# Optimization experiments

Hardware: AMD Instinct MI355X
Metric: run time of the kernel (lower is better)

## Reference

```python
import jax, jax.numpy as jnp
import numpy as np

D_MODEL = 1024
N_HEAD = 16
HEAD_DIM = D_MODEL // N_HEAD


def setup_inputs() -> dict:
    key = jax.random.key(0)
    k1, k2, k3 = jax.random.split(key, 3)
    B, T = 2, 2048
    s = 1.0 / np.sqrt(D_MODEL)
    return {
        "x": jax.random.normal(k1, (B, T, D_MODEL), dtype=jnp.float32),
        "w_qkv": jax.random.normal(k2, (D_MODEL, 3 * D_MODEL), dtype=jnp.float32) * s,
        "b_qkv": jnp.zeros((3 * D_MODEL,), dtype=jnp.float32),
        "w_out": jax.random.normal(k3, (D_MODEL, D_MODEL), dtype=jnp.float32) * s,
        "b_out": jnp.zeros((D_MODEL,), dtype=jnp.float32),
    }


def reference(x, w_qkv, b_qkv, w_out, b_out):
    B, T, C = x.shape
    qkv = x @ w_qkv + b_qkv                      # [B,T,3C]
    q, k, v = jnp.split(qkv, 3, axis=-1)
    # [B,T,C] -> [B,H,T,hd]
    def to_heads(t):
        return t.reshape(B, T, N_HEAD, HEAD_DIM).transpose(0, 2, 1, 3)
    q, k, v = to_heads(q), to_heads(k), to_heads(v)
    scale = 1.0 / np.sqrt(HEAD_DIM).astype(np.float32)
    att = jnp.einsum("bhqd,bhkd->bhqk", q, k) * scale  # [B,H,T,T]
    causal = jnp.tril(jnp.ones((T, T), dtype=bool))
    att = jnp.where(causal, att, -jnp.inf)
    att = jax.nn.softmax(att, axis=-1)
    y = jnp.einsum("bhqk,bhkd->bhqd", att, v)    # [B,H,T,hd]
    y = y.transpose(0, 2, 1, 3).reshape(B, T, C)
    return y @ w_out + b_out
```

## Files before the change

### kernel.cpp

```cpp
#include <hip/hip_runtime.h>
#include <stdint.h>

#define D_MODEL 1024
#define NHEAD 16
#define HD 64
#define BB 2
#define TT 2048
#define MR (BB*TT)

#define SCL2 0.18033688011112042f

typedef unsigned short u16;
typedef __bf16 bf16x8 __attribute__((ext_vector_type(8)));
typedef __bf16 bf16x4v __attribute__((ext_vector_type(4)));
typedef u16 u16x8 __attribute__((ext_vector_type(8)));
typedef float f32x4 __attribute__((ext_vector_type(4)));

__device__ __forceinline__ u16 f2bf(float f) {
  union { float f; unsigned u; } v; v.f = f;
  unsigned r = v.u + 0x7FFFu + ((v.u >> 16) & 1u);
  return (u16)(r >> 16);
}

__device__ __forceinline__ void gload_lds16(const void* g, void* l) {
  __builtin_amdgcn_global_load_lds(
      (const __attribute__((address_space(1))) void*)g,
      (__attribute__((address_space(3))) void*)l, 16, 0, 0);
}

__global__ void k_f32_to_bf16(const float* __restrict__ src, u16* __restrict__ dst, int n4) {
  int idx = blockIdx.x * blockDim.x + threadIdx.x;
  int stride = gridDim.x * blockDim.x;
  for (int i = idx; i < n4; i += stride) {
    float4 v = reinterpret_cast<const float4*>(src)[i];
    ushort4 o;
    o.x = f2bf(v.x); o.y = f2bf(v.y); o.z = f2bf(v.z); o.w = f2bf(v.w);
    reinterpret_cast<ushort4*>(dst)[i] = o;
  }
}

__global__ void k_transpose_both(const float* __restrict__ wqkv, const float* __restrict__ wout,
                                 u16* __restrict__ dqkv, u16* __restrict__ dout) {
  __shared__ float tile[32][33];
  int bx = blockIdx.x;
  const float* src; u16* dst; int N; int n0;
  if (bx < 96) { src = wqkv; dst = dqkv; N = 3 * D_MODEL; n0 = bx * 32; }
  else         { src = wout; dst = dout; N = D_MODEL;     n0 = (bx - 96) * 32; }
  const int K = D_MODEL;
  int k0 = blockIdx.y * 32;
  int tx = threadIdx.x, ty = threadIdx.y;
  #pragma unroll
  for (int i = 0; i < 32; i += 8)
    tile[ty + i][tx] = src[(size_t)(k0 + ty + i) * N + n0 + tx];
  __syncthreads();
  #pragma unroll
  for (int i = 0; i < 32; i += 8)
    dst[(size_t)(n0 + ty + i) * K + k0 + tx] = f2bf(tile[tx][ty + i]);
}

template<int MODE>
__global__ __launch_bounds__(256)
void k_gemm_bt(const u16* __restrict__ A, const u16* __restrict__ Bt,
               const float* __restrict__ bias,
               u16* __restrict__ q_out, u16* __restrict__ k_out, u16* __restrict__ v_out,
               float* __restrict__ c_out, int M, int N, int K)
{
  __shared__ __align__(16) u16 a_sh[128 * 64];
  __shared__ __align__(16) u16 b_sh[128 * 64];
  const int u = threadIdx.x;
  const int lane = u & 63;
  const int w = u >> 6;
  const int wr = w >> 1, wc = w & 1;
  const int m0 = blockIdx.y * 128;
  const int n0 = blockIdx.x * 128;
  const int r = lane & 15, q4 = lane >> 4;

  f32x4 acc[4][4];
  #pragma unroll
  for (int i = 0; i < 4; i++)
    #pragma unroll
    for (int j = 0; j < 4; j++) acc[i][j] = {0.f, 0.f, 0.f, 0.f};

  const int arow = u >> 3;
  const int acol = ((u & 7) ^ ((u >> 3) & 7)) * 8;
  const u16* Ag = A + (size_t)(m0 + arow) * K + acol;
  const u16* Bg = Bt + (size_t)(n0 + arow) * K + acol;

  const int fs0 = ((0 * 4 + q4) ^ (r & 7)) * 8;
  const int fs1 = ((1 * 4 + q4) ^ (r & 7)) * 8;

  for (int k0 = 0; k0 < K; k0 += 64) {
    #pragma unroll
    for (int i = 0; i < 4; i++) {
      gload_lds16(Ag + (size_t)i * 32 * K + k0, &a_sh[(i * 32 + w * 8) * 64]);
      gload_lds16(Bg + (size_t)i * 32 * K + k0, &b_sh[(i * 32 + w * 8) * 64]);
    }
    __syncthreads();
    #pragma unroll
    for (int kc = 0; kc < 2; kc++) {
      const int fs = kc ? fs1 : fs0;
      bf16x8 af[4], bfr[4];
      #pragma unroll
      for (int m = 0; m < 4; m++)
        af[m] = *reinterpret_cast<const bf16x8*>(&a_sh[(wr * 64 + m * 16 + r) * 64 + fs]);
      #pragma unroll
      for (int n = 0; n < 4; n++)
        bfr[n] = *reinterpret_cast<const bf16x8*>(&b_sh[(wc * 64 + n * 16 + r) * 64 + fs]);
      #pragma unroll
      for (int m = 0; m < 4; m++)
        #pragma unroll
        for (int n = 0; n < 4; n++)
          acc[m][n] = __builtin_amdgcn_mfma_f32_16x16x32_bf16(af[m], bfr[n], acc[m][n], 0, 0, 0);
    }
    __syncthreads();
  }

  if (MODE == 0) {
    #pragma unroll
    for (int n = 0; n < 4; n++) {
      int gcol = n0 + wc * 64 + n * 16 + r;
      int which = gcol >> 10;
      int rem = gcol & 1023;
      int h = rem >> 6, d = rem & 63;
      float bv = bias[gcol];
      #pragma unroll
      for (int m = 0; m < 4; m++) {
        #pragma unroll
        for (int reg = 0; reg < 4; reg++) {
          int grow = m0 + wr * 64 + m * 16 + q4 * 4 + reg;
          int b = grow >> 11, t = grow & 2047;
          float fv = acc[m][n][reg] + bv;
          if (which == 0)
            q_out[(((size_t)(b * NHEAD + h) * TT + t) << 6) + d] = f2bf(fv * SCL2);
          else if (which == 1)
            k_out[(((size_t)(b * NHEAD + h) * TT + t) << 6) + d] = f2bf(fv);
          else
            v_out[(((size_t)(b * NHEAD + h) * HD + d) * TT) + t] = f2bf(fv);
        }
      }
    }
  } else {
    #pragma unroll
    for (int m = 0; m < 4; m++) {
      #pragma unroll
      for (int reg = 0; reg < 4; reg++) {
        int grow = m0 + wr * 64 + m * 16 + q4 * 4 + reg;
        #pragma unroll
        for (int n = 0; n < 4; n++) {
          int gcol = n0 + wc * 64 + n * 16 + r;
          c_out[(size_t)grow * N + gcol] = acc[m][n][reg] + bias[gcol];
        }
      }
    }
  }
}

#define DEFER_THR 6.0f

__device__ __forceinline__ void attn_step(
    const u16* __restrict__ kb, const u16* __restrict__ vb,
    const bf16x8 (&qf)[2][2], f32x4 (&of)[2][4],
    float (&m_run)[2], float (&lp)[2],
    u16* pw, int kt, bool diag, int q0, int r, int q4, int fsw0, int fsw1)
{
  f32x4 sf[2][4];
  __builtin_amdgcn_s_setprio(1);
  #pragma unroll
  for (int n = 0; n < 4; n++) {
    bf16x8 k0f = *reinterpret_cast<const bf16x8*>(&kb[(n * 16 + r) * 64 + fsw0]);
    bf16x8 k1f = *reinterpret_cast<const bf16x8*>(&kb[(n * 16 + r) * 64 + fsw1]);
    #pragma unroll
    for (int g = 0; g < 2; g++) {
      f32x4 a = {0.f, 0.f, 0.f, 0.f};
      a = __builtin_amdgcn_mfma_f32_16x16x32_bf16(k0f, qf[g][0], a, 0, 0, 0);
      a = __builtin_amdgcn_mfma_f32_16x16x32_bf16(k1f, qf[g][1], a, 0, 0, 0);
      sf[g][n] = a;
    }
  }
  __builtin_amdgcn_s_setprio(0);

  bf16x8 vf[2][4];
  #pragma unroll
  for (int d0 = 0; d0 < 4; d0++) {
    vf[0][d0] = *reinterpret_cast<const bf16x8*>(&vb[(d0 * 16 + r) * 64 + fsw0]);
    vf[1][d0] = *reinterpret_cast<const bf16x8*>(&vb[(d0 * 16 + r) * 64 + fsw1]);
  }

  #pragma unroll
  for (int g = 0; g < 2; g++) {
    const int myq = q0 + g * 16 + r;
    if (diag) {
      #pragma unroll
      for (int n = 0; n < 4; n++)
        #pragma unroll
        for (int reg = 0; reg < 4; reg++) {
          int kg = kt * 64 + n * 16 + q4 * 4 + reg;
          if (kg > myq) sf[g][n][reg] = -1e30f;
        }
    }
    float ma = fmaxf(fmaxf(sf[g][0][0], sf[g][0][1]), sf[g][0][2]);
    float mb = fmaxf(fmaxf(sf[g][0][3], sf[g][1][0]), sf[g][1][1]);
    float mc = fmaxf(fmaxf(sf[g][1][2], sf[g][1][3]), sf[g][2][0]);
    float md = fmaxf(fmaxf(sf[g][2][1], sf[g][2][2]), sf[g][2][3]);
    float me = fmaxf(fmaxf(sf[g][3][0], sf[g][3][1]), sf[g][3][2]);
    float mt = fmaxf(fmaxf(fmaxf(ma, mb), fmaxf(mc, md)), fmaxf(me, sf[g][3][3]));

    if (!__all(mt <= m_run[g] + DEFER_THR)) {
      float fm = fmaxf(mt, __shfl_xor(mt, 16));
      fm = fmaxf(fm, __shfl_xor(fm, 32));
      float mnew = fmaxf(m_run[g], fm);
      float alpha = __builtin_amdgcn_exp2f(m_run[g] - mnew);
      lp[g] *= alpha;
      #pragma unroll
      for (int d0 = 0; d0 < 4; d0++)
        of[g][d0] *= alpha;
      m_run[g] = mnew;
    }

    f32x4 ss = {0.f, 0.f, 0.f, 0.f};
    #pragma unroll
    for (int n = 0; n < 4; n++) {
      #pragma unroll
      for (int reg = 0; reg < 4; reg++)
        sf[g][n][reg] = __builtin_amdgcn_exp2f(sf[g][n][reg] - m_run[g]);
      ss += sf[g][n];
    }
    lp[g] += (ss[0] + ss[1]) + (ss[2] + ss[3]);

    #pragma unroll
    for (int n = 0; n < 4; n++) {
      bf16x4v pv;
      pv[0] = (__bf16)sf[g][n][0]; pv[1] = (__bf16)sf[g][n][1];
      pv[2] = (__bf16)sf[g][n][2]; pv[3] = (__bf16)sf[g][n][3];
      *reinterpret_cast<bf16x4v*>(&pw[(g * 16 + r) * 72 + n * 16 + q4 * 4]) = pv;
    }
  }

  #pragma unroll
  for (int g = 0; g < 2; g++)
    #pragma unroll
    for (int kc = 0; kc < 2; kc++) {
      bf16x8 pa = *reinterpret_cast<const bf16x8*>(&pw[(g * 16 + r) * 72 + kc * 32 + q4 * 8]);
      #pragma unroll
      for (int d0 = 0; d0 < 4; d0++)
        of[g][d0] = __builtin_amdgcn_mfma_f32_16x16x32_bf16(vf[kc][d0], pa, of[g][d0], 0, 0, 0);
    }
}

__global__ __launch_bounds__(512)
void k_attn(const u16* __restrict__ Q, const u16* __restrict__ Kk,
            const u16* __restrict__ Vt, u16* __restrict__ Y)
{
  __shared__ __align__(16) u16 kbuf[2][64 * 64];
  __shared__ __align__(16) u16 vbuf[2][64 * 64];
  __shared__ __align__(16) u16 p_sh[8][32 * 72];

  const int u = threadIdx.x;
  const int lane = u & 63;
  const int w = u >> 6;
  const int r = lane & 15, q4 = lane >> 4;
  const int xcd = blockIdx.x & 7;
  const int j = blockIdx.x >> 3;
  const int p = j & 31;
  const int member = j >> 5;
  const int bh = xcd * 4 + (p & 3);
  const int st = member ? (p >> 2) : (15 - (p >> 2));
  const int s = w & 3;
  const int hf = w >> 2;
  const int b = bh >> 4, h = bh & 15;
  const size_t head_off = (size_t)bh * TT * HD;
  const int q0 = st * 128 + s * 32;
  const int NTh = st + 1;
  const int ktmax = q0 >> 6;

  const int srow = w * 8 + (lane >> 3);
  const int sg = (lane & 7) ^ (srow & 7);
  const u16* Ksrc = Kk + head_off + (size_t)srow * HD + sg * 8;
  const u16* Vsrc = Vt + head_off + (size_t)srow * TT + sg * 8;

  bf16x8 qf[2][2];
  #pragma unroll
  for (int g = 0; g < 2; g++) {
    const u16* qp = &Q[head_off + (size_t)(q0 + g * 16 + r) * HD + q4 * 8];
    qf[g][0] = *reinterpret_cast<const bf16x8*>(qp);
    qf[g][1] = *reinterpret_cast<const bf16x8*>(qp + 32);
  }

  f32x4 of[2][4];
  #pragma unroll
  for (int g = 0; g < 2; g++)
    #pragma unroll
    for (int k = 0; k < 4; k++) of[g][k] = {0.f, 0.f, 0.f, 0.f};
  float m_run[2] = {-1e30f, -1e30f};
  float lp[2] = {0.f, 0.f};

  u16* pw = &p_sh[w][0];
  const int fsw0 = ((0 * 4 + q4) ^ (r & 7)) * 8;
  const int fsw1 = ((1 * 4 + q4) ^ (r & 7)) * 8;

  for (int i = 0; i < NTh; i++) {
    gload_lds16(Ksrc + (size_t)i * (64 * HD),          &kbuf[0][w * 512]);
    gload_lds16(Vsrc + i * 64,                         &vbuf[0][w * 512]);
    gload_lds16(Ksrc + (size_t)(i + NTh) * (64 * HD),  &kbuf[1][w * 512]);
    gload_lds16(Vsrc + (i + NTh) * 64,                 &vbuf[1][w * 512]);
    __syncthreads();
    const int kt = i + hf * NTh;
    if (kt <= ktmax)
      attn_step(&kbuf[hf][0], &vbuf[hf][0], qf, of, m_run, lp, pw,
                kt, kt == ktmax, q0, r, q4, fsw0, fsw1);
    __syncthreads();
  }

  float* msh = reinterpret_cast<float*>(&p_sh[0][0]);
  if (hf == 1) {
    float* mb = msh + (s * 36) * 64 + lane;
    #pragma unroll
    for (int g = 0; g < 2; g++) {
      #pragma unroll
      for (int d0 = 0; d0 < 4; d0++)
        #pragma unroll
        for (int jj = 0; jj < 4; jj++)
          mb[(g * 16 + d0 * 4 + jj) * 64] = of[g][d0][jj];
      mb[(32 + g) * 64] = m_run[g];
      mb[(34 + g) * 64] = lp[g];
    }
  }
  __syncthreads();
  if (hf == 0) {
    const float* mb = msh + (s * 36) * 64 + lane;
    #pragma unroll
    for (int g = 0; g < 2; g++) {
      float m1 = mb[(32 + g) * 64];
      float l1 = mb[(34 + g) * 64];
      float M = fmaxf(m_run[g], m1);
      float a0 = __builtin_amdgcn_exp2f(m_run[g] - M);
      float a1 = __builtin_amdgcn_exp2f(m1 - M);
      float lc = lp[g] * a0 + l1 * a1;
      lc += __shfl_xor(lc, 16);
      lc += __shfl_xor(lc, 32);
      float inv = 1.0f / lc;
      const int t = q0 + g * 16 + r;
      #pragma unroll
      for (int d0 = 0; d0 < 4; d0++) {
        f32x4 oc;
        #pragma unroll
        for (int jj = 0; jj < 4; jj++)
          oc[jj] = of[g][d0][jj] * a0 + mb[(g * 16 + d0 * 4 + jj) * 64] * a1;
        bf16x4v yv;
        yv[0] = (__bf16)(oc[0] * inv); yv[1] = (__bf16)(oc[1] * inv);
        yv[2] = (__bf16)(oc[2] * inv); yv[3] = (__bf16)(oc[3] * inv);
        *reinterpret_cast<bf16x4v*>(&Y[((size_t)(b * TT + t) << 10) + h * 64 + d0 * 16 + q4 * 4]) = yv;
      }
    }
  }
}

extern "C" void kernel_launch(void* const* d_in, const int* in_sizes, int n_in,
                              void* d_out, int out_size, void* d_ws, size_t ws_size,
                              hipStream_t stream) {
  const float* x     = (const float*)d_in[0];
  const float* w_qkv = (const float*)d_in[1];
  const float* b_qkv = (const float*)d_in[2];
  const float* w_out = (const float*)d_in[3];
  const float* b_out = (const float*)d_in[4];
  float* out = (float*)d_out;

  uint8_t* ws = (uint8_t*)d_ws;
  u16* xb    = (u16*)(ws);
  u16* wqkvT = (u16*)(ws + (8u  << 20));
  u16* woutT = (u16*)(ws + (14u << 20));
  u16* Qh    = (u16*)(ws + (16u << 20));
  u16* Kh    = (u16*)(ws + (24u << 20));
  u16* Vth   = (u16*)(ws + (32u << 20));

  k_f32_to_bf16<<<1024, 256, 0, stream>>>(x, xb, (MR * D_MODEL) / 4);
  k_transpose_both<<<dim3(128, D_MODEL / 32), dim3(32, 8), 0, stream>>>(
      w_qkv, w_out, wqkvT, woutT);

  k_gemm_bt<0><<<dim3(3 * D_MODEL / 128, MR / 128), 256, 0, stream>>>(
      xb, wqkvT, b_qkv, Qh, Kh, Vth, nullptr, MR, 3 * D_MODEL, D_MODEL);

  u16* Yh = xb;
  k_attn<<<dim3(512), dim3(512), 0, stream>>>(Qh, Kh, Vth, Yh);

  k_gemm_bt<1><<<dim3(D_MODEL / 128, MR / 128), 256, 0, stream>>>(
      Yh, woutT, b_out, nullptr, nullptr, nullptr, out, MR, D_MODEL, D_MODEL);
}
```

Before: 123.2 us.

## Split attention into 64-row query blocks and narrow output GEMM tiles

The attention kernel goes from 512 blocks of 512 threads, each covering 128 query rows with paired tiles, to 1024 blocks of 256 threads, each covering 64 query rows. The key range of each block is split into two halves handled by different wave pairs. The output projection gets its own kernel with 128x64 tiles, which doubles its block count from 256 to 512 so more CUs are busy on the 1024-wide GEMM. The finer split is meant to improve load balance and occupancy, at the cost of more blocks, more K/V reloads per query row, and possibly uneven causal work between the two halves.

```diff
diff --git a/kernel.cpp b/kernel.cpp
--- a/kernel.cpp
+++ b/kernel.cpp
@@ -58,12 +58,11 @@
     dst[(size_t)(n0 + ty + i) * K + k0 + tx] = f2bf(tile[tx][ty + i]);
 }
 
-template<int MODE>
 __global__ __launch_bounds__(256)
-void k_gemm_bt(const u16* __restrict__ A, const u16* __restrict__ Bt,
-               const float* __restrict__ bias,
-               u16* __restrict__ q_out, u16* __restrict__ k_out, u16* __restrict__ v_out,
-               float* __restrict__ c_out, int M, int N, int K)
+void k_gemm_qkv(const u16* __restrict__ A, const u16* __restrict__ Bt,
+                const float* __restrict__ bias,
+                u16* __restrict__ q_out, u16* __restrict__ k_out, u16* __restrict__ v_out,
+                int M, int N, int K)
 {
   __shared__ __align__(16) u16 a_sh[128 * 64];
   __shared__ __align__(16) u16 b_sh[128 * 64];
@@ -115,41 +114,95 @@
     __syncthreads();
   }
 
-  if (MODE == 0) {
-    #pragma unroll
-    for (int n = 0; n < 4; n++) {
-      int gcol = n0 + wc * 64 + n * 16 + r;
-      int which = gcol >> 10;
-      int rem = gcol & 1023;
-      int h = rem >> 6, d = rem & 63;
-      float bv = bias[gcol];
-      #pragma unroll
-      for (int m = 0; m < 4; m++) {
-        #pragma unroll
-        for (int reg = 0; reg < 4; reg++) {
-          int grow = m0 + wr * 64 + m * 16 + q4 * 4 + reg;
-          int b = grow >> 11, t = grow & 2047;
-          float fv = acc[m][n][reg] + bv;
-          if (which == 0)
-            q_out[(((size_t)(b * NHEAD + h) * TT + t) << 6) + d] = f2bf(fv * SCL2);
-          else if (which == 1)
-            k_out[(((size_t)(b * NHEAD + h) * TT + t) << 6) + d] = f2bf(fv);
-          else
-            v_out[(((size_t)(b * NHEAD + h) * HD + d) * TT) + t] = f2bf(fv);
-        }
-      }
-    }
-  } else {
+  #pragma unroll
+  for (int n = 0; n < 4; n++) {
+    int gcol = n0 + wc * 64 + n * 16 + r;
+    int which = gcol >> 10;
+    int rem = gcol & 1023;
+    int h = rem >> 6, d = rem & 63;
+    float bv = bias[gcol];
     #pragma unroll
     for (int m = 0; m < 4; m++) {
       #pragma unroll
       for (int reg = 0; reg < 4; reg++) {
         int grow = m0 + wr * 64 + m * 16 + q4 * 4 + reg;
+        int b = grow >> 11, t = grow & 2047;
+        float fv = acc[m][n][reg] + bv;
+        if (which == 0)
+          q_out[(((size_t)(b * NHEAD + h) * TT + t) << 6) + d] = f2bf(fv * SCL2);
+        else if (which == 1)
+          k_out[(((size_t)(b * NHEAD + h) * TT + t) << 6) + d] = f2bf(fv);
+        else
+          v_out[(((size_t)(b * NHEAD + h) * HD + d) * TT) + t] = f2bf(fv);
+      }
+    }
+  }
+}
+
+__global__ __launch_bounds__(256)
+void k_gemm_out(const u16* __restrict__ A, const u16* __restrict__ Bt,
+                const float* __restrict__ bias, float* __restrict__ c_out,
+                int M, int N, int K)
+{
+  __shared__ __align__(16) u16 a_sh[128 * 64];
+  __shared__ __align__(16) u16 b_sh[64 * 64];
+  const int u = threadIdx.x;
+  const int lane = u & 63;
+  const int w = u >> 6;
+  const int m0 = blockIdx.y * 128;
+  const int n0 = blockIdx.x * 64;
+  const int r = lane & 15, q4 = lane >> 4;
+
+  f32x4 acc[2][4];
+  #pragma unroll
+  for (int i = 0; i < 2; i++)
+    #pragma unroll
+    for (int j = 0; j < 4; j++) acc[i][j] = {0.f, 0.f, 0.f, 0.f};
+
+  const int arow = u >> 3;
+  const int acol = ((u & 7) ^ ((u >> 3) & 7)) * 8;
+  const u16* Ag = A + (size_t)(m0 + arow) * K + acol;
+  const u16* Bg = Bt + (size_t)(n0 + arow) * K + acol;
+
+  const int fs0 = ((0 * 4 + q4) ^ (r & 7)) * 8;
+  const int fs1 = ((1 * 4 + q4) ^ (r & 7)) * 8;
+
+  for (int k0 = 0; k0 < K; k0 += 64) {
+    #pragma unroll
+    for (int i = 0; i < 4; i++)
+      gload_lds16(Ag + (size_t)i * 32 * K + k0, &a_sh[(i * 32 + w * 8) * 64]);
+    #pragma unroll
+    for (int i = 0; i < 2; i++)
+      gload_lds16(Bg + (size_t)i * 32 * K + k0, &b_sh[(i * 32 + w * 8) * 64]);
+    __syncthreads();
+    #pragma unroll
+    for (int kc = 0; kc < 2; kc++) {
+      const int fs = kc ? fs1 : fs0;
+      bf16x8 af[2], bfr[4];
+      #pragma unroll
+      for (int m = 0; m < 2; m++)
+        af[m] = *reinterpret_cast<const bf16x8*>(&a_sh[(w * 32 + m * 16 + r) * 64 + fs]);
+      #pragma unroll
+      for (int n = 0; n < 4; n++)
+        bfr[n] = *reinterpret_cast<const bf16x8*>(&b_sh[(n * 16 + r) * 64 + fs]);
+      #pragma unroll
+      for (int m = 0; m < 2; m++)
         #pragma unroll
-        for (int n = 0; n < 4; n++) {
-          int gcol = n0 + wc * 64 + n * 16 + r;
-          c_out[(size_t)grow * N + gcol] = acc[m][n][reg] + bias[gcol];
-        }
+        for (int n = 0; n < 4; n++)
+          acc[m][n] = __builtin_amdgcn_mfma_f32_16x16x32_bf16(af[m], bfr[n], acc[m][n], 0, 0, 0);
+    }
+    __syncthreads();
+  }
+
+  #pragma unroll
+  for (int m = 0; m < 2; m++) {
+    #pragma unroll
+    for (int reg = 0; reg < 4; reg++) {
+      int grow = m0 + w * 32 + m * 16 + q4 * 4 + reg;
+      #pragma unroll
+      for (int n = 0; n < 4; n++) {
+        int gcol = n0 + n * 16 + r;
+        c_out[(size_t)grow * N + gcol] = acc[m][n][reg] + bias[gcol];
       }
     }
   }
@@ -247,13 +300,13 @@
     }
 }
 
-__global__ __launch_bounds__(512)
+__global__ __launch_bounds__(256)
 void k_attn(const u16* __restrict__ Q, const u16* __restrict__ Kk,
             const u16* __restrict__ Vt, u16* __restrict__ Y)
 {
   __shared__ __align__(16) u16 kbuf[2][64 * 64];
   __shared__ __align__(16) u16 vbuf[2][64 * 64];
-  __shared__ __align__(16) u16 p_sh[8][32 * 72];
+  __shared__ __align__(16) u16 p_sh[4][32 * 72];
 
   const int u = threadIdx.x;
   const int lane = u & 63;
@@ -261,19 +314,18 @@
   const int r = lane & 15, q4 = lane >> 4;
   const int xcd = blockIdx.x & 7;
   const int j = blockIdx.x >> 3;
-  const int p = j & 31;
-  const int member = j >> 5;
-  const int bh = xcd * 4 + (p & 3);
-  const int st = member ? (p >> 2) : (15 - (p >> 2));
-  const int s = w & 3;
-  const int hf = w >> 2;
+  const int bh = xcd * 4 + (j & 3);
+  const int s64 = 31 - (j >> 2);
+  const int s = w & 1;
+  const int hf = w >> 1;
   const int b = bh >> 4, h = bh & 15;
   const size_t head_off = (size_t)bh * TT * HD;
-  const int q0 = st * 128 + s * 32;
-  const int NTh = st + 1;
-  const int ktmax = q0 >> 6;
-
-  const int srow = w * 8 + (lane >> 3);
+  const int q0 = s64 * 64 + s * 32;
+  const int NT = s64 + 1;
+  const int NTh = (NT + 1) >> 1;
+  const int ktmax = s64;
+
+  const int srow = w * 16 + (lane >> 3);
   const int sg = (lane & 7) ^ (srow & 7);
   const u16* Ksrc = Kk + head_off + (size_t)srow * HD + sg * 8;
   const u16* Vsrc = Vt + head_off + (size_t)srow * TT + sg * 8;
@@ -299,13 +351,18 @@
   const int fsw1 = ((1 * 4 + q4) ^ (r & 7)) * 8;
 
   for (int i = 0; i < NTh; i++) {
-    gload_lds16(Ksrc + (size_t)i * (64 * HD),          &kbuf[0][w * 512]);
-    gload_lds16(Vsrc + i * 64,                         &vbuf[0][w * 512]);
-    gload_lds16(Ksrc + (size_t)(i + NTh) * (64 * HD),  &kbuf[1][w * 512]);
-    gload_lds16(Vsrc + (i + NTh) * 64,                 &vbuf[1][w * 512]);
+    const int t1 = NTh + i;
+    gload_lds16(Ksrc + (size_t)i  * (64 * HD),          &kbuf[0][(w * 16) * 64]);
+    gload_lds16(Ksrc + (size_t)i  * (64 * HD) + 8 * HD, &kbuf[0][(w * 16 + 8) * 64]);
+    gload_lds16(Ksrc + (size_t)t1 * (64 * HD),          &kbuf[1][(w * 16) * 64]);
+    gload_lds16(Ksrc + (size_t)t1 * (64 * HD) + 8 * HD, &kbuf[1][(w * 16 + 8) * 64]);
+    gload_lds16(Vsrc + i * 64,                          &vbuf[0][(w * 16) * 64]);
+    gload_lds16(Vsrc + i * 64 + 8 * TT,                 &vbuf[0][(w * 16 + 8) * 64]);
+    gload_lds16(Vsrc + t1 * 64,                         &vbuf[1][(w * 16) * 64]);
+    gload_lds16(Vsrc + t1 * 64 + 8 * TT,                &vbuf[1][(w * 16 + 8) * 64]);
     __syncthreads();
     const int kt = i + hf * NTh;
-    if (kt <= ktmax)
+    if (kt < NT)
       attn_step(&kbuf[hf][0], &vbuf[hf][0], qf, of, m_run, lp, pw,
                 kt, kt == ktmax, q0, r, q4, fsw0, fsw1);
     __syncthreads();
@@ -377,12 +434,12 @@
   k_transpose_both<<<dim3(128, D_MODEL / 32), dim3(32, 8), 0, stream>>>(
       w_qkv, w_out, wqkvT, woutT);
 
-  k_gemm_bt<0><<<dim3(3 * D_MODEL / 128, MR / 128), 256, 0, stream>>>(
-      xb, wqkvT, b_qkv, Qh, Kh, Vth, nullptr, MR, 3 * D_MODEL, D_MODEL);
+  k_gemm_qkv<<<dim3(3 * D_MODEL / 128, MR / 128), 256, 0, stream>>>(
+      xb, wqkvT, b_qkv, Qh, Kh, Vth, MR, 3 * D_MODEL, D_MODEL);
 
   u16* Yh = xb;
-  k_attn<<<dim3(512), dim3(512), 0, stream>>>(Qh, Kh, Vth, Yh);
-
-  k_gemm_bt<1><<<dim3(D_MODEL / 128, MR / 128), 256, 0, stream>>>(
-      Yh, woutT, b_out, nullptr, nullptr, nullptr, out, MR, D_MODEL, D_MODEL);
-}
+  k_attn<<<dim3(1024), dim3(256), 0, stream>>>(Qh, Kh, Vth, Yh);
+
+  k_gemm_out<<<dim3(D_MODEL / 64, MR / 128), 256, 0, stream>>>(
+      Yh, woutT, b_out, out, MR, D_MODEL, D_MODEL);
+}
```

New measurement: 114.5 us. -7.0%, faster.
